# Optimization experiments

Hardware: AMD Instinct MI355X
Metric: run time of the kernel (lower is better)

The kernel has to match this reference:

```python
import jax, jax.numpy as jnp
import numpy as np

B, H, S, DK = 2, 16, 2048, 64


def setup_inputs() -> dict:
    key = jax.random.key(0)
    kq, kk, kv = jax.random.split(key, 3)
    query = jax.random.normal(kq, (B, H, S, DK), dtype=jnp.float32)
    k = jax.random.normal(kk, (B, H, S, DK), dtype=jnp.float32)
    value = jax.random.normal(kv, (B, H, S, DK), dtype=jnp.float32)
    # causal padding-style mask: 1 = keep, 0 = masked (set to -inf pre-softmax)
    mask = jnp.tril(jnp.ones((S, S), dtype=jnp.int32))[None, None, :, :]
    return {"query": query, "key": k, "value": value, "d_k": DK, "mask": mask}


def reference(query, key, value, d_k, mask):
    # scores: [B, H, Sq, Sk]
    scores = jnp.einsum("bhqd,bhkd->bhqk", query, key)
    scores = scores / jnp.sqrt(jnp.asarray(d_k, dtype=scores.dtype))
    scores = jnp.where(mask == 0, -jnp.inf, scores)
    att = jax.nn.softmax(scores, axis=-1)
    # dropout is identity in eval mode (deterministic reference)
    out = jnp.einsum("bhqk,bhkd->bhqd", att, value)
    return out
```

## Files before the change

### kernel.cpp

```cpp
#include <hip/hip_runtime.h>
#include <cstdint>

#define B_ 2
#define H_ 16
#define S_ 2048
#define DK_ 64
#define BH_ (B_*H_)
#define NQT 32

typedef __attribute__((ext_vector_type(8))) short short8;
typedef __attribute__((ext_vector_type(4))) short short4v;
typedef __attribute__((ext_vector_type(4))) float floatx4;

__device__ inline unsigned short f2bf(float f) {
  union { float f; unsigned u; } v; v.f = f;
  unsigned u = v.u;
  unsigned r = u + 0x7fffu + ((u >> 16) & 1u);
  return (unsigned short)(r >> 16);
}

__device__ inline floatx4 mfma16(short4v a, short4v b, floatx4 c) {
#if __has_builtin(__builtin_amdgcn_mfma_f32_16x16x16bf16_1k)
  return __builtin_amdgcn_mfma_f32_16x16x16bf16_1k(a, b, c, 0, 0, 0);
#else
  asm("v_mfma_f32_16x16x16_bf16 %0, %1, %2, %0" : "+v"(c) : "v"(a), "v"(b));
  return c;
#endif
}

__device__ inline short4v u2s4(unsigned a, unsigned b) {
  union { unsigned u[2]; short4v s; } v;
  v.u[0] = a; v.u[1] = b;
  return v.s;
}

__global__ __launch_bounds__(256) void conv_kv(const float* __restrict__ K,
                                               const float* __restrict__ V,
                                               unsigned short* __restrict__ Kb,
                                               unsigned short* __restrict__ Vb) {
  __shared__ __align__(16) unsigned short t[64 * 80];
  const int bh = blockIdx.y, s0 = blockIdx.x * 64;
  const int row = threadIdx.x >> 2, cp = threadIdx.x & 3;

  {
    const float* src = K + ((size_t)(bh * S_ + s0 + row)) * DK_ + cp * 16;
    unsigned short* dst = Kb + ((size_t)(bh * S_ + s0 + row)) * DK_ + cp * 16;
    #pragma unroll
    for (int h = 0; h < 2; ++h) {
      float4 a = *(const float4*)(src + h * 8);
      float4 b = *(const float4*)(src + h * 8 + 4);
      uint4 st;
      st.x = (unsigned)f2bf(a.x) | ((unsigned)f2bf(a.y) << 16);
      st.y = (unsigned)f2bf(a.z) | ((unsigned)f2bf(a.w) << 16);
      st.z = (unsigned)f2bf(b.x) | ((unsigned)f2bf(b.y) << 16);
      st.w = (unsigned)f2bf(b.z) | ((unsigned)f2bf(b.w) << 16);
      *(uint4*)(dst + h * 8) = st;
    }
  }
  {
    const float* src = V + ((size_t)(bh * S_ + s0 + row)) * DK_ + cp * 16;
    #pragma unroll
    for (int j4 = 0; j4 < 4; ++j4) {
      float4 a = *(const float4*)(src + j4 * 4);
      int c = cp * 16 + j4 * 4;
      t[(c + 0) * 80 + row] = f2bf(a.x);
      t[(c + 1) * 80 + row] = f2bf(a.y);
      t[(c + 2) * 80 + row] = f2bf(a.z);
      t[(c + 3) * 80 + row] = f2bf(a.w);
    }
    __syncthreads();
    unsigned short* dst = Vb + ((size_t)(bh * DK_ + row)) * S_ + s0 + cp * 16;
    *(uint4*)(dst + 0) = *(const uint4*)&t[row * 80 + cp * 16];
    *(uint4*)(dst + 8) = *(const uint4*)&t[row * 80 + cp * 16 + 8];
  }
}

__global__ __launch_bounds__(256, 3)
void fa_kernel(const float* __restrict__ Q, const unsigned short* __restrict__ Kb,
               const unsigned short* __restrict__ Vb, float* __restrict__ Out) {
  __shared__ __align__(16) unsigned short SMEM[6 * 4096];

  const int tid  = threadIdx.x;
  const int wave = tid >> 6;
  const int lane = tid & 63;
  const int quad = lane >> 4;
  const int l16  = lane & 15;

  const int id = blockIdx.x;
  const int bh = (id & 7) | (((id >> 3) & 3) << 3);
  const int qt = NQT - 1 - (id >> 5);
  const int nkv = qt + 1;

  const float SCL = 0.125f * 1.44269504088896340736f;

  short8 qf[8];
  #pragma unroll
  for (int nq = 0; nq < 4; ++nq) {
    const float* p = Q + ((size_t)bh * S_ + qt * 64 + nq * 16 + l16) * DK_ + quad * 8;
    #pragma unroll
    for (int ks = 0; ks < 2; ++ks) {
      float4 x = *(const float4*)(p + ks * 32);
      float4 y = *(const float4*)(p + ks * 32 + 4);
      short8 t;
      t[0]=(short)f2bf(x.x*SCL); t[1]=(short)f2bf(x.y*SCL); t[2]=(short)f2bf(x.z*SCL); t[3]=(short)f2bf(x.w*SCL);
      t[4]=(short)f2bf(y.x*SCL); t[5]=(short)f2bf(y.y*SCL); t[6]=(short)f2bf(y.z*SCL); t[7]=(short)f2bf(y.w*SCL);
      qf[nq * 2 + ks] = t;
    }
  }

  floatx4 Ot[4][4];
  float ls[4] = {0.f, 0.f, 0.f, 0.f};
  #pragma unroll
  for (int d = 0; d < 4; ++d)
    #pragma unroll
    for (int nq = 0; nq < 4; ++nq) Ot[d][nq] = (floatx4){0,0,0,0};

  auto stage = [&](int buf, int kv) {
    unsigned short* Ktb = SMEM + buf * 4096;
    unsigned short* Vtb = SMEM + (3 + buf) * 4096;
    #pragma unroll
    for (int rd = 0; rd < 2; ++rd) {
      const int cid = rd * 256 + wave * 64 + lane;
      const int row = cid >> 3;
      const int c   = (cid & 7) ^ (row & 7);
      {
        const unsigned short* g = Kb + (((size_t)bh * S_ + kv * 64 + row) << 6) + (c << 3);
        __builtin_amdgcn_global_load_lds(
            (const __attribute__((address_space(1))) void*)g,
            (__attribute__((address_space(3))) void*)&Ktb[(rd * 4 + wave) * 512], 16, 0, 0);
      }
      {
        const unsigned short* g = Vb + (((size_t)(bh * DK_ + row)) << 11) + kv * 64 + (c << 3);
        __builtin_amdgcn_global_load_lds(
            (const __attribute__((address_space(1))) void*)g,
            (__attribute__((address_space(3))) void*)&Vtb[(rd * 4 + wave) * 512], 16, 0, 0);
      }
    }
  };

  auto computeT = [&](int cur, bool last) {
    const unsigned short* Ktc = SMEM + cur * 4096;
    const unsigned short* Vtc = SMEM + (3 + cur) * 4096;
    const int rk = wave * 16 + l16;
    const short8 ck0 = *(const short8*)&Ktc[rk * 64 + ((quad    ) ^ (l16 & 7)) * 8];
    const short8 ck1 = *(const short8*)&Ktc[rk * 64 + ((quad + 4) ^ (l16 & 7)) * 8];
    short4v cv[4];
    #pragma unroll
    for (int dblk = 0; dblk < 4; ++dblk)
      cv[dblk] = *(const short4v*)&Vtc[(dblk * 16 + l16) * 64 +
                    ((wave * 2 + (quad >> 1)) ^ (l16 & 7)) * 8 + (quad & 1) * 4];
    unsigned pk[4][2];
    #pragma unroll
    for (int nq = 0; nq < 4; ++nq) {
      if (last && nq < wave) continue;
      floatx4 s0 = (floatx4){0,0,0,0};
      __builtin_amdgcn_s_setprio(1);
      s0 = __builtin_amdgcn_mfma_f32_16x16x32_bf16(ck0, qf[nq * 2 + 0], s0, 0, 0, 0);
      s0 = __builtin_amdgcn_mfma_f32_16x16x32_bf16(ck1, qf[nq * 2 + 1], s0, 0, 0, 0);
      __builtin_amdgcn_s_setprio(0);
      if (last && nq == wave) {
        #pragma unroll
        for (int r = 0; r < 4; ++r)
          if (quad * 4 + r > l16) s0[r] = -INFINITY;
      }
      float e0 = __builtin_amdgcn_exp2f(s0[0]);
      float e1 = __builtin_amdgcn_exp2f(s0[1]);
      float e2 = __builtin_amdgcn_exp2f(s0[2]);
      float e3 = __builtin_amdgcn_exp2f(s0[3]);
      ls[nq] += (e0 + e1) + (e2 + e3);
      pk[nq][0] = __builtin_amdgcn_perm(__float_as_uint(e1) + 0x8000u,
                                        __float_as_uint(e0) + 0x8000u, 0x07060302u);
      pk[nq][1] = __builtin_amdgcn_perm(__float_as_uint(e3) + 0x8000u,
                                        __float_as_uint(e2) + 0x8000u, 0x07060302u);
    }
    __builtin_amdgcn_s_setprio(1);
    #pragma unroll
    for (int nq = 0; nq < 4; ++nq) {
      if (last && nq < wave) continue;
      const short4v pb = u2s4(pk[nq][0], pk[nq][1]);
      Ot[0][nq] = mfma16(cv[0], pb, Ot[0][nq]);
      Ot[1][nq] = mfma16(cv[1], pb, Ot[1][nq]);
      Ot[2][nq] = mfma16(cv[2], pb, Ot[2][nq]);
      Ot[3][nq] = mfma16(cv[3], pb, Ot[3][nq]);
    }
    __builtin_amdgcn_s_setprio(0);
  };

  stage(0, 0);
  if (nkv > 1) stage(1, 1);
  int cur = 0;
  for (int kv = 0; kv < nkv; ++kv) {
    if (kv + 1 < nkv) asm volatile("s_waitcnt vmcnt(4)" ::: "memory");
    else              asm volatile("s_waitcnt vmcnt(0)" ::: "memory");
    __builtin_amdgcn_s_barrier();
    if (kv + 2 < nkv) stage(cur == 0 ? 2 : cur - 1, kv + 2);
    computeT(cur, kv == nkv - 1);
    cur = (cur == 2) ? 0 : cur + 1;
  }

  floatx4* OredV = (floatx4*)SMEM;
  float*   Lred  = (float*)SMEM + 8192;
  #pragma unroll
  for (int nq = 0; nq < 4; ++nq) {
    ls[nq] += __shfl_xor(ls[nq], 16);
    ls[nq] += __shfl_xor(ls[nq], 32);
  }
  __syncthreads();
  if (lane < 16) {
    #pragma unroll
    for (int nq = 0; nq < 4; ++nq) Lred[(wave * 4 + nq) * 16 + lane] = ls[nq];
  }
  float inv = 0.f;
  #pragma unroll
  for (int rnd = 0; rnd < 2; ++rnd) {
    #pragma unroll
    for (int db = 0; db < 2; ++db)
      #pragma unroll
      for (int nq = 0; nq < 4; ++nq)
        OredV[((wave * 2 + db) * 4 + nq) * 64 + lane] = Ot[rnd * 2 + db][nq];
    __syncthreads();
    if (rnd == 0) {
      const float lt = Lred[(0 * 4 + wave) * 16 + l16] + Lred[(1 * 4 + wave) * 16 + l16]
                     + Lred[(2 * 4 + wave) * 16 + l16] + Lred[(3 * 4 + wave) * 16 + l16];
      inv = 1.0f / lt;
    }
    #pragma unroll
    for (int db = 0; db < 2; ++db) {
      floatx4 s = OredV[((0 * 2 + db) * 4 + wave) * 64 + lane]
                + OredV[((1 * 2 + db) * 4 + wave) * 64 + lane]
                + OredV[((2 * 2 + db) * 4 + wave) * 64 + lane]
                + OredV[((3 * 2 + db) * 4 + wave) * 64 + lane];
      s *= inv;
      *(floatx4*)(Out + ((size_t)(bh * S_ + qt * 64 + wave * 16 + l16)) * 64
                      + (rnd * 2 + db) * 16 + quad * 4) = s;
    }
    if (rnd == 0) __syncthreads();
  }
}

extern "C" void kernel_launch(void* const* d_in, const int* in_sizes, int n_in,
                              void* d_out, int out_size, void* d_ws, size_t ws_size,
                              hipStream_t stream) {
  const float* Q = (const float*)d_in[0];
  const float* K = (const float*)d_in[1];
  const float* V = (const float*)d_in[2];
  float* Out = (float*)d_out;
  unsigned short* Kb = (unsigned short*)d_ws;
  unsigned short* Vb = Kb + (size_t)BH_ * S_ * DK_;
  conv_kv<<<dim3(S_ / 64, BH_), 256, 0, stream>>>(K, V, Kb, Vb);
  fa_kernel<<<dim3(NQT * BH_), 256, 0, stream>>>(Q, Kb, Vb, Out);
}
```

Measured before the change: 144.5 us.

## Give each wave private K/V tiles to drop per-iteration block barriers

Each wave now loads only the 16 key rows and matching V columns it consumes into its own double-buffered LDS region. The per-iteration s_barrier goes away, and the triple-buffer pipeline becomes a per-wave double buffer that prefetches one tile ahead. LDS per block shrinks, which could allow more resident blocks. In exchange the prefetch depth is shorter and the V swizzle is simpler, so LDS bank conflicts or exposed load latency may grow. There is also a hazard: with no barrier, the reduction epilogue that reuses SMEM relies on the __syncthreads that follows.

Result: no change. 142.1 us (-1.7%).

```diff
diff --git a/kernel.cpp b/kernel.cpp
--- a/kernel.cpp
+++ b/kernel.cpp
@@ -78,7 +78,7 @@
 __global__ __launch_bounds__(256, 3)
 void fa_kernel(const float* __restrict__ Q, const unsigned short* __restrict__ Kb,
                const unsigned short* __restrict__ Vb, float* __restrict__ Out) {
-  __shared__ __align__(16) unsigned short SMEM[6 * 4096];
+  __shared__ __align__(16) unsigned short SMEM[4 * 4096 + 512];
 
   const int tid  = threadIdx.x;
   const int wave = tid >> 6;
@@ -115,40 +115,42 @@
     #pragma unroll
     for (int nq = 0; nq < 4; ++nq) Ot[d][nq] = (floatx4){0,0,0,0};
 
-  auto stage = [&](int buf, int kv) {
-    unsigned short* Ktb = SMEM + buf * 4096;
-    unsigned short* Vtb = SMEM + (3 + buf) * 4096;
-    #pragma unroll
-    for (int rd = 0; rd < 2; ++rd) {
-      const int cid = rd * 256 + wave * 64 + lane;
-      const int row = cid >> 3;
-      const int c   = (cid & 7) ^ (row & 7);
+  auto stage = [&](int slot, int kv) {
+    unsigned short* base = SMEM + wave * 4096 + slot * 2048;
+    #pragma unroll
+    for (int j = 0; j < 2; ++j) {
+      const int kap = 64 * j + lane;
       {
-        const unsigned short* g = Kb + (((size_t)bh * S_ + kv * 64 + row) << 6) + (c << 3);
+        const int r = kap >> 3;
+        const int c = (kap & 7) ^ (r & 7);
+        const unsigned short* g =
+            Kb + (((size_t)(bh * S_ + kv * 64 + wave * 16 + r)) << 6) + (c << 3);
         __builtin_amdgcn_global_load_lds(
             (const __attribute__((address_space(1))) void*)g,
-            (__attribute__((address_space(3))) void*)&Ktb[(rd * 4 + wave) * 512], 16, 0, 0);
+            (__attribute__((address_space(3))) void*)(base + j * 512), 16, 0, 0);
       }
       {
-        const unsigned short* g = Vb + (((size_t)(bh * DK_ + row)) << 11) + kv * 64 + (c << 3);
+        const int d = kap >> 1;
+        const int h = (kap & 1) ^ ((kap >> 1) & 1);
+        const unsigned short* g =
+            Vb + (((size_t)(bh * DK_ + d)) << 11) + kv * 64 + wave * 16 + h * 8;
         __builtin_amdgcn_global_load_lds(
             (const __attribute__((address_space(1))) void*)g,
-            (__attribute__((address_space(3))) void*)&Vtb[(rd * 4 + wave) * 512], 16, 0, 0);
+            (__attribute__((address_space(3))) void*)(base + 1024 + j * 512), 16, 0, 0);
       }
     }
   };
 
-  auto computeT = [&](int cur, bool last) {
-    const unsigned short* Ktc = SMEM + cur * 4096;
-    const unsigned short* Vtc = SMEM + (3 + cur) * 4096;
-    const int rk = wave * 16 + l16;
-    const short8 ck0 = *(const short8*)&Ktc[rk * 64 + ((quad    ) ^ (l16 & 7)) * 8];
-    const short8 ck1 = *(const short8*)&Ktc[rk * 64 + ((quad + 4) ^ (l16 & 7)) * 8];
+  auto computeT = [&](int slot, bool last) {
+    const unsigned short* kb_ = SMEM + wave * 4096 + slot * 2048;
+    const unsigned short* vb_ = kb_ + 1024;
+    const short8 ck0 = *(const short8*)&kb_[l16 * 64 + ((quad    ) ^ (l16 & 7)) * 8];
+    const short8 ck1 = *(const short8*)&kb_[l16 * 64 + ((quad + 4) ^ (l16 & 7)) * 8];
     short4v cv[4];
     #pragma unroll
     for (int dblk = 0; dblk < 4; ++dblk)
-      cv[dblk] = *(const short4v*)&Vtc[(dblk * 16 + l16) * 64 +
-                    ((wave * 2 + (quad >> 1)) ^ (l16 & 7)) * 8 + (quad & 1) * 4];
+      cv[dblk] = *(const short4v*)&vb_[(dblk * 16 + l16) * 16 +
+                    (((quad >> 1) ^ (l16 & 1)) * 8) + (quad & 1) * 4];
     unsigned pk[4][2];
     #pragma unroll
     for (int nq = 0; nq < 4; ++nq) {
@@ -187,19 +189,19 @@
   };
 
   stage(0, 0);
-  if (nkv > 1) stage(1, 1);
-  int cur = 0;
   for (int kv = 0; kv < nkv; ++kv) {
-    if (kv + 1 < nkv) asm volatile("s_waitcnt vmcnt(4)" ::: "memory");
-    else              asm volatile("s_waitcnt vmcnt(0)" ::: "memory");
-    __builtin_amdgcn_s_barrier();
-    if (kv + 2 < nkv) stage(cur == 0 ? 2 : cur - 1, kv + 2);
-    computeT(cur, kv == nkv - 1);
-    cur = (cur == 2) ? 0 : cur + 1;
+    const int slot = kv & 1;
+    if (kv + 1 < nkv) {
+      stage(slot ^ 1, kv + 1);
+      asm volatile("s_waitcnt vmcnt(4)" ::: "memory");
+    } else {
+      asm volatile("s_waitcnt vmcnt(0)" ::: "memory");
+    }
+    computeT(slot, kv == nkv - 1);
   }
 
   floatx4* OredV = (floatx4*)SMEM;
-  float*   Lred  = (float*)SMEM + 8192;
+  float*   Lred  = (float*)(SMEM + 4 * 4096);
   #pragma unroll
   for (int nq = 0; nq < 4; ++nq) {
     ls[nq] += __shfl_xor(ls[nq], 16);
```
